# Kernel tuning notes

Hardware: AMD Instinct MI355X
Metric: run time of the kernel (lower is better)

The kernel has to match this reference:

```python
import jax, jax.numpy as jnp
import numpy as np

B, S, HID = 2, 1024, 2048
H, HK, D = 32, 4, 128
G = H // HK
EPS = 1e-6
SCALE = 1.0 / np.sqrt(D)
ROPE_THETA = 1000000.0


def _rope_tables(seq_len, dim, theta):
    inv_freq = 1.0 / (theta ** (np.arange(0, dim, 2, dtype=np.float32) / dim))
    t = np.arange(seq_len, dtype=np.float32)
    freqs = np.outer(t, inv_freq)                      # [S, D/2]
    emb = np.concatenate([freqs, freqs], axis=-1)       # [S, D]
    return (jnp.asarray(np.cos(emb))[None, :, None, :],
            jnp.asarray(np.sin(emb))[None, :, None, :])  # [1,S,1,D]


def setup_inputs() -> dict:
    key = jax.random.key(0)
    k1, k2, k3 = jax.random.split(key, 3)
    cos, sin = _rope_tables(S, D, ROPE_THETA)
    return {
        "hidden_states": jax.random.normal(k1, (B, S, HID), jnp.float32),
        "cos": cos,
        "sin": sin,
        "w_qkv": jax.random.normal(k2, (HID, (H + 2 * HK) * D), jnp.float32) * 0.02,
        "q_norm_w": jnp.ones((D,), jnp.float32),
        "k_norm_w": jnp.ones((D,), jnp.float32),
        "w_o": jax.random.normal(k3, (H * D, HID), jnp.float32) * 0.02,
    }


def _rms_norm(x, w):
    xf = x.astype(jnp.float32)
    var = jnp.mean(xf * xf, axis=-1, keepdims=True)
    return (w * (xf * jax.lax.rsqrt(var + EPS))).astype(x.dtype)


def _rotate_half(x):
    x1, x2 = jnp.split(x, 2, axis=-1)
    return jnp.concatenate([-x2, x1], axis=-1)


def reference(hidden_states, cos, sin, w_qkv, q_norm_w, k_norm_w, w_o):
    b, s, _ = hidden_states.shape
    qkv = hidden_states @ w_qkv                          # [B,S,(H+2HK)*D]
    q, k, v = jnp.split(qkv, [H * D, (H + HK) * D], axis=-1)
    q = q.reshape(b, s, H, D)
    k = k.reshape(b, s, HK, D)
    v = v.reshape(b, s, HK, D)
    # per-head RMSNorm on q/k, then rotary (BSH layout)
    q = _rms_norm(q, q_norm_w)
    k = _rms_norm(k, k_norm_w)
    q = q * cos + _rotate_half(q) * sin
    k = k * cos + _rotate_half(k) * sin
    # grouped-query causal SDPA (prefill path, sparse_mode=2)
    qg = q.reshape(b, s, HK, G, D)
    scores = jnp.einsum("bqkgd,bskd->bkgqs", qg, k) * SCALE  # [B,HK,G,S,S]
    causal = jnp.tril(jnp.ones((s, s), bool))
    scores = jnp.where(causal, scores, jnp.finfo(scores.dtype).min)
    probs = jax.nn.softmax(scores, axis=-1)
    ctx = jnp.einsum("bkgqs,bskd->bqkgd", probs, v)          # [B,S,HK,G,D]
    ctx = ctx.reshape(b, s, H * D)
    return ctx @ w_o                                          # [B,S,HID]
```

## Files before the change

### kernel.cpp

```cpp
#include <hip/hip_runtime.h>

#define B_   2
#define S_   1024
#define HID_ 2048
#define H_   32
#define HK_  4
#define D_   128
#define NQKV ((H_ + 2 * HK_) * D_)
#define TOK  (B_ * S_)

typedef short bf16x8  __attribute__((ext_vector_type(8)));
typedef short short4v __attribute__((ext_vector_type(4)));
typedef float f32x4   __attribute__((ext_vector_type(4)));
typedef int   i32x4   __attribute__((ext_vector_type(4)));

__device__ inline short f2bf(float f) {
  unsigned u = __builtin_bit_cast(unsigned, f);
  u += 0x7fffu + ((u >> 16) & 1u);
  return (short)(u >> 16);
}
__device__ inline float bf2f(short s) {
  return __builtin_bit_cast(float, ((unsigned)(unsigned short)s) << 16);
}

__device__ __forceinline__ void gld_lds16(const short* g, short* l) {
  __builtin_amdgcn_global_load_lds((__attribute__((address_space(1))) void*)g,
                                   (__attribute__((address_space(3))) void*)l, 16, 0, 0);
}

__global__ __launch_bounds__(256) void cast_f32_bf16(const float* __restrict__ in,
                                                     short* __restrict__ out, int n4) {
  int i = blockIdx.x * 256 + threadIdx.x;
  if (i >= n4) return;
  f32x4 v = ((const f32x4*)in)[i];
  short4v o;
  o[0] = f2bf(v[0]); o[1] = f2bf(v[1]); o[2] = f2bf(v[2]); o[3] = f2bf(v[3]);
  ((short4v*)out)[i] = o;
}

__global__ __launch_bounds__(256) void transpose_cast(const float* __restrict__ in,
                                                      short* __restrict__ out,
                                                      int K, int N) {
  __shared__ float tile[32][33];
  int nb = blockIdx.x * 32, kb = blockIdx.y * 32;
  int c = threadIdx.x & 31, r0 = threadIdx.x >> 5;
#pragma unroll
  for (int i = 0; i < 4; i++) {
    int r = r0 + i * 8;
    tile[r][c] = in[(size_t)(kb + r) * N + nb + c];
  }
  __syncthreads();
#pragma unroll
  for (int i = 0; i < 4; i++) {
    int r = r0 + i * 8;
    out[(size_t)(nb + r) * K + kb + c] = f2bf(tile[c][r]);
  }
}

__global__ __launch_bounds__(256) void gemm_bt128(const short* __restrict__ A,
                                                  const short* __restrict__ Bt,
                                                  float* __restrict__ C,
                                                  int M, int N, int Kfull, int klen) {
  const int tid  = threadIdx.x;
  const int m0   = blockIdx.y * 128;
  const int n0   = blockIdx.x * 128;
  const int kz0  = blockIdx.z * klen;
  const int w    = tid >> 6, lane = tid & 63;
  const int quad = lane >> 4, l16 = lane & 15;
  const int wm   = (w >> 1) * 64, wn = (w & 1) * 64;

  __shared__ short As[128 * 64];
  __shared__ short Bs[128 * 64];

  const f32x4 z = {0.f, 0.f, 0.f, 0.f};
  f32x4 acc[4][4];
#pragma unroll
  for (int i = 0; i < 4; i++)
#pragma unroll
    for (int j = 0; j < 4; j++) acc[i][j] = z;

  const int srow = lane >> 3;
  const int lc   = (lane & 7) ^ srow;

  for (int kk = 0; kk < klen; kk += 64) {
    const int k0 = kz0 + kk;
#pragma unroll
    for (int i = 0; i < 4; i++) {
      int rb = w * 32 + i * 8;
      gld_lds16(&A [(size_t)(m0 + rb + srow) * Kfull + k0 + lc * 8], &As[rb * 64]);
      gld_lds16(&Bt[(size_t)(n0 + rb + srow) * Kfull + k0 + lc * 8], &Bs[rb * 64]);
    }
    __syncthreads();
#pragma unroll
    for (int kb = 0; kb < 2; kb++) {
      const int pc = ((kb * 4 + quad) ^ (l16 & 7)) * 8;
      bf16x8 a[4], b[4];
#pragma unroll
      for (int f = 0; f < 4; f++) {
        a[f] = *(const bf16x8*)&As[(wm + f * 16 + l16) * 64 + pc];
        b[f] = *(const bf16x8*)&Bs[(wn + f * 16 + l16) * 64 + pc];
      }
#pragma unroll
      for (int fi = 0; fi < 4; fi++)
#pragma unroll
        for (int fj = 0; fj < 4; fj++)
          acc[fi][fj] = __builtin_amdgcn_mfma_f32_16x16x32_bf16(a[fi], b[fj], acc[fi][fj], 0, 0, 0);
    }
    __syncthreads();
  }

  float* Cz = C + (size_t)blockIdx.z * M * N;
#pragma unroll
  for (int fi = 0; fi < 4; fi++) {
    int row0 = m0 + wm + fi * 16 + quad * 4;
#pragma unroll
    for (int fj = 0; fj < 4; fj++) {
      int col = n0 + wn + fj * 16 + l16;
#pragma unroll
      for (int r = 0; r < 4; r++)
        Cz[(size_t)(row0 + r) * N + col] = acc[fi][fj][r];
    }
  }
}

__global__ __launch_bounds__(256) void add2(const float* __restrict__ a,
                                            const float* __restrict__ b,
                                            float* __restrict__ c, int n4) {
  int i = blockIdx.x * 256 + threadIdx.x;
  if (i >= n4) return;
  f32x4 va = ((const f32x4*)a)[i], vb = ((const f32x4*)b)[i];
  ((f32x4*)c)[i] = va + vb;
}

__global__ __launch_bounds__(256, 4) void gemm_qkv(const short* __restrict__ A,
                                                   const short* __restrict__ Bt,
                                                   const float* __restrict__ cosT,
                                                   const float* __restrict__ sinT,
                                                   const float* __restrict__ qw,
                                                   const float* __restrict__ kw,
                                                   short* __restrict__ Qb,
                                                   short* __restrict__ Kb,
                                                   short* __restrict__ Vt) {
  const int tid  = threadIdx.x;
  const int m0   = blockIdx.y * 64;
  const int n0   = blockIdx.x * 128;
  const int w    = tid >> 6, lane = tid & 63;
  const int quad = lane >> 4, l16 = lane & 15;
  const int wm   = (w >> 1) * 32, wn = (w & 1) * 64;

  __shared__ short As[64 * 64];
  __shared__ short Bs[128 * 64];
  __shared__ float ss_lds[4][32];

  const f32x4 z = {0.f, 0.f, 0.f, 0.f};
  f32x4 acc[2][4];
#pragma unroll
  for (int i = 0; i < 2; i++)
#pragma unroll
    for (int j = 0; j < 4; j++) acc[i][j] = z;

  const int srow = lane >> 3;
  const int lc   = (lane & 7) ^ srow;

  for (int k0 = 0; k0 < HID_; k0 += 64) {
#pragma unroll
    for (int i = 0; i < 2; i++) {
      int rb = w * 16 + i * 8;
      gld_lds16(&A[(size_t)(m0 + rb + srow) * HID_ + k0 + lc * 8], &As[rb * 64]);
    }
#pragma unroll
    for (int i = 0; i < 4; i++) {
      int rb = w * 32 + i * 8;
      gld_lds16(&Bt[(size_t)(n0 + rb + srow) * HID_ + k0 + lc * 8], &Bs[rb * 64]);
    }
    __syncthreads();
#pragma unroll
    for (int kb = 0; kb < 2; kb++) {
      const int pc = ((kb * 4 + quad) ^ (l16 & 7)) * 8;
      bf16x8 a[2], b[4];
#pragma unroll
      for (int f = 0; f < 2; f++)
        a[f] = *(const bf16x8*)&As[(wm + f * 16 + l16) * 64 + pc];
#pragma unroll
      for (int f = 0; f < 4; f++)
        b[f] = *(const bf16x8*)&Bs[(wn + f * 16 + l16) * 64 + pc];
#pragma unroll
      for (int fi = 0; fi < 2; fi++)
#pragma unroll
        for (int fj = 0; fj < 4; fj++)
          acc[fi][fj] = __builtin_amdgcn_mfma_f32_16x16x32_bf16(a[fi], b[fj], acc[fi][fj], 0, 0, 0);
    }
    __syncthreads();
  }

  const int hd = n0 >> 7;
  const int bb = m0 >> 10;
  const int sW = (m0 & (S_ - 1)) + wm;

  if (hd >= H_ + HK_) {
    const int khv = hd - (H_ + HK_);
    short* dstV = Vt + ((size_t)(bb * HK_ + khv) * D_) * S_;
#pragma unroll
    for (int fi = 0; fi < 2; fi++) {
      int s = sW + fi * 16 + quad * 4;
#pragma unroll
      for (int fj = 0; fj < 4; fj++) {
        int d = wn + fj * 16 + l16;
        short4v o;
#pragma unroll
        for (int r = 0; r < 4; r++) o[r] = f2bf(acc[fi][fj][r]);
        *(short4v*)&dstV[(size_t)d * S_ + s] = o;
      }
    }
    return;
  }

  float ssp[2][4];
#pragma unroll
  for (int fi = 0; fi < 2; fi++)
#pragma unroll
    for (int r = 0; r < 4; r++) {
      float t = 0.f;
#pragma unroll
      for (int fj = 0; fj < 4; fj++) t += acc[fi][fj][r] * acc[fi][fj][r];
      ssp[fi][r] = t;
    }
#pragma unroll
  for (int off = 1; off < 16; off <<= 1)
#pragma unroll
    for (int fi = 0; fi < 2; fi++)
#pragma unroll
      for (int r = 0; r < 4; r++) ssp[fi][r] += __shfl_xor(ssp[fi][r], off, 64);
  if (l16 == 0)
#pragma unroll
    for (int fi = 0; fi < 2; fi++)
#pragma unroll
      for (int r = 0; r < 4; r++) ss_lds[w][fi * 16 + quad * 4 + r] = ssp[fi][r];
  __syncthreads();
  float rn[2][4];
#pragma unroll
  for (int fi = 0; fi < 2; fi++)
#pragma unroll
    for (int r = 0; r < 4; r++) {
      int row = fi * 16 + quad * 4 + r;
      rn[fi][r] = rsqrtf((ss_lds[w][row] + ss_lds[w ^ 1][row]) * (1.0f / 128.0f) + 1e-6f);
    }
  const float* wv = (hd < H_) ? qw : kw;
  float wgt[4];
#pragma unroll
  for (int fj = 0; fj < 4; fj++) wgt[fj] = wv[wn + fj * 16 + l16];

  short* xown = ((w & 1) ? Bs : As) + (w >> 1) * 2048;
  short* xpar = ((w & 1) ? As : Bs) + (w >> 1) * 2048;
#pragma unroll
  for (int fi = 0; fi < 2; fi++)
#pragma unroll
    for (int fj = 0; fj < 4; fj++) {
      short4v y4;
#pragma unroll
      for (int r = 0; r < 4; r++) y4[r] = f2bf(acc[fi][fj][r] * rn[fi][r] * wgt[fj]);
      *(short4v*)&xown[(((fi * 4 + fj) * 4 + quad) * 16 + l16) * 4] = y4;
    }
  __syncthreads();

  const float sign = (wn == 0) ? -1.0f : 1.0f;
  const float osc  = (hd < H_) ? (0.08838834764831845f * 1.4426950408889634f) : 1.0f;
  short* dstQ = (hd < H_) ? (Qb + (((size_t)bb * H_ + hd) * S_) * D_)
                          : (Kb + (((size_t)bb * HK_ + (hd - H_)) * S_) * D_);
#pragma unroll
  for (int fi = 0; fi < 2; fi++)
#pragma unroll
    for (int fj = 0; fj < 4; fj++) {
      short4v yp4 = *(const short4v*)&xpar[(((fi * 4 + fj) * 4 + quad) * 16 + l16) * 4];
      int d = wn + fj * 16 + l16;
#pragma unroll
      for (int r = 0; r < 4; r++) {
        int s = sW + fi * 16 + quad * 4 + r;
        float y  = acc[fi][fj][r] * rn[fi][r] * wgt[fj];
        float yp = bf2f(yp4[r]);
        float c  = cosT[s * D_ + d];
        float sn = sinT[s * D_ + d];
        dstQ[(size_t)s * D_ + d] = f2bf((y * c + sign * yp * sn) * osc);
      }
    }
}

__global__ __launch_bounds__(256) void attn_mfma5(const short* __restrict__ Qb,
                                                  const short* __restrict__ Kb,
                                                  const short* __restrict__ Vt,
                                                  short* __restrict__ ctx) {
  const int qmap[8] = {7, 0, 6, 1, 5, 2, 4, 3};
  const int qt = qmap[blockIdx.x & 7];
  const int h  = blockIdx.y;
  const int b  = blockIdx.z;
  const int kh = h >> 3;
  const int q0 = qt * 128;
  const int tid = threadIdx.x, w = tid >> 6, lane = tid & 63;
  const int quad = lane >> 4, l16 = lane & 15;
  const float MBIAS = 18.0f;

  __shared__ short Ks[128 * 64];
  __shared__ short Vs[144 * 64];
  __shared__ short Ps[4][2][16 * 72];

  for (int i = tid; i < 16 * 64; i += 256) Vs[128 * 64 + i] = (short)0x3F80;

  const short* Qbase = Qb + (((size_t)b * H_ + h) * S_ + q0) * D_;
  bf16x8 aq[2][4];
#pragma unroll
  for (int fi = 0; fi < 2; fi++)
#pragma unroll
    for (int kb = 0; kb < 4; kb++)
      aq[fi][kb] = *(const bf16x8*)&Qbase[(size_t)(fi * 64 + w * 16 + l16) * D_ + kb * 32 + quad * 8];

  const f32x4 z = {0.f, 0.f, 0.f, 0.f};
  f32x4 O[2][9];
#pragma unroll
  for (int fi = 0; fi < 2; fi++)
#pragma unroll
    for (int n = 0; n < 9; n++) O[fi][n] = z;

  const short* Kbase = Kb + ((size_t)(b * HK_ + kh) * S_) * D_;
  const short* Vbase = Vt + ((size_t)(b * HK_ + kh) * D_) * S_;

  const int srow = lane >> 3;
  const int lc   = (lane & 7) ^ srow;

  const int nkt = 2 * qt + 2;
  for (int kt = 0; kt < nkt; kt++) {
    const int k0 = kt * 64;
    __syncthreads();
#pragma unroll
    for (int i = 0; i < 4; i++) {
      int rb = w * 32 + i * 8;
      int rr = rb + srow;
      gld_lds16(&Kbase[(size_t)(k0 + (rr & 63)) * D_ + (rr >> 6) * 64 + lc * 8], &Ks[rb * 64]);
      gld_lds16(&Vbase[(size_t)rr * S_ + k0 + lc * 8], &Vs[rb * 64]);
    }
    __syncthreads();

#pragma unroll
    for (int nb = 0; nb < 4; nb++) {
      f32x4 s0 = z, s1 = z;
#pragma unroll
      for (int kb = 0; kb < 4; kb++) {
        const int c  = kb * 4 + quad;
        const int c7 = c & 7;
        const int rr = (c >> 3) * 64 + nb * 16 + l16;
        bf16x8 bk = *(const bf16x8*)&Ks[rr * 64 + (c7 ^ (l16 & 7)) * 8];
        s0 = __builtin_amdgcn_mfma_f32_16x16x32_bf16(aq[0][kb], bk, s0, 0, 0, 0);
        s1 = __builtin_amdgcn_mfma_f32_16x16x32_bf16(aq[1][kb], bk, s1, 0, 0, 0);
      }
      const int col = k0 + nb * 16 + l16;
#pragma unroll
      for (int r = 0; r < 4; r++) {
        int row0 = q0 + w * 16 + quad * 4 + r;
        float p0 = (col > row0) ? 0.0f : exp2f(s0[r] - MBIAS);
        float p1 = (col > row0 + 64) ? 0.0f : exp2f(s1[r] - MBIAS);
        Ps[w][0][(quad * 4 + r) * 72 + nb * 16 + l16] = f2bf(p0);
        Ps[w][1][(quad * 4 + r) * 72 + nb * 16 + l16] = f2bf(p1);
      }
    }

#pragma unroll
    for (int kb2 = 0; kb2 < 2; kb2++) {
      bf16x8 ap0 = *(const bf16x8*)&Ps[w][0][l16 * 72 + kb2 * 32 + quad * 8];
      bf16x8 ap1 = *(const bf16x8*)&Ps[w][1][l16 * 72 + kb2 * 32 + quad * 8];
      const int c7 = kb2 * 4 + quad;
#pragma unroll
      for (int nb2 = 0; nb2 < 9; nb2++) {
        int d = nb2 * 16 + l16;
        bf16x8 bv = *(const bf16x8*)&Vs[d * 64 + (c7 ^ (d & 7)) * 8];
        O[0][nb2] = __builtin_amdgcn_mfma_f32_16x16x32_bf16(ap0, bv, O[0][nb2], 0, 0, 0);
        O[1][nb2] = __builtin_amdgcn_mfma_f32_16x16x32_bf16(ap1, bv, O[1][nb2], 0, 0, 0);
      }
    }
  }

#pragma unroll
  for (int fi = 0; fi < 2; fi++)
#pragma unroll
    for (int r = 0; r < 4; r++) {
      float inv = 1.0f / O[fi][8][r];
      size_t row = (size_t)(b * S_ + q0 + fi * 64 + w * 16 + quad * 4 + r);
      short* dst = ctx + row * (H_ * D_) + h * D_;
#pragma unroll
      for (int nb2 = 0; nb2 < 8; nb2++)
        dst[nb2 * 16 + l16] = f2bf(O[fi][nb2][r] * inv);
    }
}

extern "C" void kernel_launch(void* const* d_in, const int* in_sizes, int n_in,
                              void* d_out, int out_size, void* d_ws, size_t ws_size,
                              hipStream_t stream) {
  (void)in_sizes; (void)n_in; (void)out_size; (void)ws_size;
  const float* hidden = (const float*)d_in[0];
  const float* cosT   = (const float*)d_in[1];
  const float* sinT   = (const float*)d_in[2];
  const float* wqkv   = (const float*)d_in[3];
  const float* qnw    = (const float*)d_in[4];
  const float* knw    = (const float*)d_in[5];
  const float* wo     = (const float*)d_in[6];
  float* out = (float*)d_out;

  char* ws = (char*)d_ws;
  short* Qb  = (short*)ws;
  short* Kb  = (short*)(ws + 16777216);
  short* Vt  = (short*)(ws + 16777216 + 2097152);
  short* hb  = (short*)(ws + 41943040);
  short* wT  = (short*)(ws + 41943040 + 8388608);
  short* ctx = (short*)(ws + 41943040 + 8388608 + 20971520);
  float* part = (float*)ws;

  cast_f32_bf16<<<4096, 256, 0, stream>>>(hidden, hb, TOK * HID_ / 4);
  transpose_cast<<<dim3(NQKV / 32, HID_ / 32), 256, 0, stream>>>(wqkv, wT, HID_, NQKV);
  gemm_qkv<<<dim3(NQKV / 128, TOK / 64), 256, 0, stream>>>(hb, wT, cosT, sinT, qnw, knw, Qb, Kb, Vt);
  attn_mfma5<<<dim3(S_ / 128, H_, B_), 256, 0, stream>>>(Qb, Kb, Vt, ctx);
  transpose_cast<<<dim3(HID_ / 32, (H_ * D_) / 32), 256, 0, stream>>>(wo, wT, H_ * D_, HID_);
  gemm_bt128<<<dim3(HID_ / 128, TOK / 128, 2), 256, 0, stream>>>(ctx, wT, part, TOK, HID_, H_ * D_, (H_ * D_) / 2);
  add2<<<(TOK * HID_ / 4 + 255) / 256, 256, 0, stream>>>(part, part + (size_t)TOK * HID_, out, TOK * HID_ / 4);
}
```

Baseline: 321.7 us.

## Double-buffer LDS tiles in QKV and output GEMMs, shrink output tile to 64x128

Both GEMM kernels now use two LDS buffers so the next K-tile's global-to-LDS load is issued before the MFMA work on the current tile. A single vmcnt wait and barrier per iteration replaces the two syncthreads. The output projection GEMM also moves from a 128x128 to a 64x128 tile with launch bounds of 4 blocks, doubling the grid for more parallelism. The cost is doubled LDS use per block, which may reduce occupancy, and the epilogue exchange buffer in gemm_qkv is remapped onto the As array.

```diff
diff --git a/kernel.cpp b/kernel.cpp
--- a/kernel.cpp
+++ b/kernel.cpp
@@ -57,61 +57,79 @@
   }
 }
 
-__global__ __launch_bounds__(256) void gemm_bt128(const short* __restrict__ A,
-                                                  const short* __restrict__ Bt,
-                                                  float* __restrict__ C,
-                                                  int M, int N, int Kfull, int klen) {
+__global__ __launch_bounds__(256, 4) void gemm_bt64(const short* __restrict__ A,
+                                                    const short* __restrict__ Bt,
+                                                    float* __restrict__ C,
+                                                    int M, int N, int Kfull, int klen) {
   const int tid  = threadIdx.x;
-  const int m0   = blockIdx.y * 128;
+  const int m0   = blockIdx.y * 64;
   const int n0   = blockIdx.x * 128;
   const int kz0  = blockIdx.z * klen;
   const int w    = tid >> 6, lane = tid & 63;
   const int quad = lane >> 4, l16 = lane & 15;
-  const int wm   = (w >> 1) * 64, wn = (w & 1) * 64;
-
-  __shared__ short As[128 * 64];
-  __shared__ short Bs[128 * 64];
+  const int wm   = (w >> 1) * 32, wn = (w & 1) * 64;
+
+  __shared__ short As[2][64 * 64];
+  __shared__ short Bs[2][128 * 64];
 
   const f32x4 z = {0.f, 0.f, 0.f, 0.f};
-  f32x4 acc[4][4];
-#pragma unroll
-  for (int i = 0; i < 4; i++)
+  f32x4 acc[2][4];
+#pragma unroll
+  for (int i = 0; i < 2; i++)
 #pragma unroll
     for (int j = 0; j < 4; j++) acc[i][j] = z;
 
   const int srow = lane >> 3;
   const int lc   = (lane & 7) ^ srow;
-
-  for (int kk = 0; kk < klen; kk += 64) {
-    const int k0 = kz0 + kk;
-#pragma unroll
-    for (int i = 0; i < 4; i++) {
-      int rb = w * 32 + i * 8;
-      gld_lds16(&A [(size_t)(m0 + rb + srow) * Kfull + k0 + lc * 8], &As[rb * 64]);
-      gld_lds16(&Bt[(size_t)(n0 + rb + srow) * Kfull + k0 + lc * 8], &Bs[rb * 64]);
-    }
-    __syncthreads();
+  const int nt   = klen / 64;
+
+#define STAGE_O(t_) do {                                                               \
+    short* dA_ = &As[(t_) & 1][0];  short* dB_ = &Bs[(t_) & 1][0];                     \
+    const int k0_ = kz0 + (t_) * 64;                                                   \
+    _Pragma("unroll")                                                                  \
+    for (int i_ = 0; i_ < 2; i_++) {                                                   \
+      int rb_ = w * 16 + i_ * 8;                                                       \
+      gld_lds16(&A[(size_t)(m0 + rb_ + srow) * Kfull + k0_ + lc * 8], dA_ + rb_ * 64); \
+    }                                                                                  \
+    _Pragma("unroll")                                                                  \
+    for (int i_ = 0; i_ < 4; i_++) {                                                   \
+      int rb_ = w * 32 + i_ * 8;                                                       \
+      gld_lds16(&Bt[(size_t)(n0 + rb_ + srow) * Kfull + k0_ + lc * 8], dB_ + rb_ * 64);\
+    }                                                                                  \
+  } while (0)
+
+  STAGE_O(0);
+  asm volatile("s_waitcnt vmcnt(0)" ::: "memory");
+  __builtin_amdgcn_s_barrier();
+
+  for (int t = 0; t < nt; t++) {
+    if (t + 1 < nt) STAGE_O(t + 1);
+    const short* Ac = &As[t & 1][0];
+    const short* Bc = &Bs[t & 1][0];
 #pragma unroll
     for (int kb = 0; kb < 2; kb++) {
       const int pc = ((kb * 4 + quad) ^ (l16 & 7)) * 8;
-      bf16x8 a[4], b[4];
-#pragma unroll
-      for (int f = 0; f < 4; f++) {
-        a[f] = *(const bf16x8*)&As[(wm + f * 16 + l16) * 64 + pc];
-        b[f] = *(const bf16x8*)&Bs[(wn + f * 16 + l16) * 64 + pc];
-      }
-#pragma unroll
-      for (int fi = 0; fi < 4; fi++)
+      bf16x8 a[2], b[4];
+#pragma unroll
+      for (int f = 0; f < 2; f++)
+        a[f] = *(const bf16x8*)&Ac[(wm + f * 16 + l16) * 64 + pc];
+#pragma unroll
+      for (int f = 0; f < 4; f++)
+        b[f] = *(const bf16x8*)&Bc[(wn + f * 16 + l16) * 64 + pc];
+#pragma unroll
+      for (int fi = 0; fi < 2; fi++)
 #pragma unroll
         for (int fj = 0; fj < 4; fj++)
           acc[fi][fj] = __builtin_amdgcn_mfma_f32_16x16x32_bf16(a[fi], b[fj], acc[fi][fj], 0, 0, 0);
     }
-    __syncthreads();
-  }
+    asm volatile("s_waitcnt vmcnt(0)" ::: "memory");
+    __builtin_amdgcn_s_barrier();
+  }
+#undef STAGE_O
 
   float* Cz = C + (size_t)blockIdx.z * M * N;
 #pragma unroll
-  for (int fi = 0; fi < 4; fi++) {
+  for (int fi = 0; fi < 2; fi++) {
     int row0 = m0 + wm + fi * 16 + quad * 4;
 #pragma unroll
     for (int fj = 0; fj < 4; fj++) {
@@ -148,8 +166,8 @@
   const int quad = lane >> 4, l16 = lane & 15;
   const int wm   = (w >> 1) * 32, wn = (w & 1) * 64;
 
-  __shared__ short As[64 * 64];
-  __shared__ short Bs[128 * 64];
+  __shared__ short As[2][64 * 64];
+  __shared__ short Bs[2][128 * 64];
   __shared__ float ss_lds[4][32];
 
   const f32x4 z = {0.f, 0.f, 0.f, 0.f};
@@ -162,36 +180,49 @@
   const int srow = lane >> 3;
   const int lc   = (lane & 7) ^ srow;
 
-  for (int k0 = 0; k0 < HID_; k0 += 64) {
-#pragma unroll
-    for (int i = 0; i < 2; i++) {
-      int rb = w * 16 + i * 8;
-      gld_lds16(&A[(size_t)(m0 + rb + srow) * HID_ + k0 + lc * 8], &As[rb * 64]);
-    }
-#pragma unroll
-    for (int i = 0; i < 4; i++) {
-      int rb = w * 32 + i * 8;
-      gld_lds16(&Bt[(size_t)(n0 + rb + srow) * HID_ + k0 + lc * 8], &Bs[rb * 64]);
-    }
-    __syncthreads();
+#define STAGE_Q(t_) do {                                                               \
+    short* dA_ = &As[(t_) & 1][0];  short* dB_ = &Bs[(t_) & 1][0];                     \
+    const int k0_ = (t_) * 64;                                                         \
+    _Pragma("unroll")                                                                  \
+    for (int i_ = 0; i_ < 2; i_++) {                                                   \
+      int rb_ = w * 16 + i_ * 8;                                                       \
+      gld_lds16(&A[(size_t)(m0 + rb_ + srow) * HID_ + k0_ + lc * 8], dA_ + rb_ * 64);  \
+    }                                                                                  \
+    _Pragma("unroll")                                                                  \
+    for (int i_ = 0; i_ < 4; i_++) {                                                   \
+      int rb_ = w * 32 + i_ * 8;                                                       \
+      gld_lds16(&Bt[(size_t)(n0 + rb_ + srow) * HID_ + k0_ + lc * 8], dB_ + rb_ * 64); \
+    }                                                                                  \
+  } while (0)
+
+  STAGE_Q(0);
+  asm volatile("s_waitcnt vmcnt(0)" ::: "memory");
+  __builtin_amdgcn_s_barrier();
+
+  for (int t = 0; t < HID_ / 64; t++) {
+    if (t + 1 < HID_ / 64) STAGE_Q(t + 1);
+    const short* Ac = &As[t & 1][0];
+    const short* Bc = &Bs[t & 1][0];
 #pragma unroll
     for (int kb = 0; kb < 2; kb++) {
       const int pc = ((kb * 4 + quad) ^ (l16 & 7)) * 8;
       bf16x8 a[2], b[4];
 #pragma unroll
       for (int f = 0; f < 2; f++)
-        a[f] = *(const bf16x8*)&As[(wm + f * 16 + l16) * 64 + pc];
+        a[f] = *(const bf16x8*)&Ac[(wm + f * 16 + l16) * 64 + pc];
 #pragma unroll
       for (int f = 0; f < 4; f++)
-        b[f] = *(const bf16x8*)&Bs[(wn + f * 16 + l16) * 64 + pc];
+        b[f] = *(const bf16x8*)&Bc[(wn + f * 16 + l16) * 64 + pc];
 #pragma unroll
       for (int fi = 0; fi < 2; fi++)
 #pragma unroll
         for (int fj = 0; fj < 4; fj++)
           acc[fi][fj] = __builtin_amdgcn_mfma_f32_16x16x32_bf16(a[fi], b[fj], acc[fi][fj], 0, 0, 0);
     }
-    __syncthreads();
-  }
+    asm volatile("s_waitcnt vmcnt(0)" ::: "memory");
+    __builtin_amdgcn_s_barrier();
+  }
+#undef STAGE_Q
 
   const int hd = n0 >> 7;
   const int bb = m0 >> 10;
@@ -250,8 +281,9 @@
 #pragma unroll
   for (int fj = 0; fj < 4; fj++) wgt[fj] = wv[wn + fj * 16 + l16];
 
-  short* xown = ((w & 1) ? Bs : As) + (w >> 1) * 2048;
-  short* xpar = ((w & 1) ? As : Bs) + (w >> 1) * 2048;
+  short* exch = &As[0][0];
+  short* xown = exch + w * 2048;
+  short* xpar = exch + (w ^ 1) * 2048;
 #pragma unroll
   for (int fi = 0; fi < 2; fi++)
 #pragma unroll
@@ -417,6 +449,6 @@
   gemm_qkv<<<dim3(NQKV / 128, TOK / 64), 256, 0, stream>>>(hb, wT, cosT, sinT, qnw, knw, Qb, Kb, Vt);
   attn_mfma5<<<dim3(S_ / 128, H_, B_), 256, 0, stream>>>(Qb, Kb, Vt, ctx);
   transpose_cast<<<dim3(HID_ / 32, (H_ * D_) / 32), 256, 0, stream>>>(wo, wT, H_ * D_, HID_);
-  gemm_bt128<<<dim3(HID_ / 128, TOK / 128, 2), 256, 0, stream>>>(ctx, wT, part, TOK, HID_, H_ * D_, (H_ * D_) / 2);
+  gemm_bt64<<<dim3(HID_ / 128, TOK / 64, 2), 256, 0, stream>>>(ctx, wT, part, TOK, HID_, H_ * D_, (H_ * D_) / 2);
   add2<<<(TOK * HID_ / 4 + 255) / 256, 256, 0, stream>>>(part, part + (size_t)TOK * HID_, out, TOK * HID_ / 4);
 }
```

Result: no change. 324.2 us (+0.8%).
